# Performance work log

Hardware: AMD Instinct MI355X
Metric: run time of the kernel (lower is better)

The kernel has to match this reference:

```python
import jax, jax.numpy as jnp
import numpy as np


def setup_inputs() -> dict:
    key = jax.random.key(0)
    ks = jax.random.split(key, 8)
    B, M, C, H, W = 2, 16, 256, 64, 64
    T = 1024  # transformer_dim
    return {
        "transformer_output": jax.random.normal(ks[0], (B, T), dtype=jnp.float32),
        "residual_maps": jax.random.normal(ks[1], (B, M, C, H, W), dtype=jnp.float32),
        "Wq": jax.random.normal(ks[2], (C, T), dtype=jnp.float32) * 0.02,
        "bq": jnp.zeros((C,), dtype=jnp.float32),
        "Wk": jax.random.normal(ks[3], (C, C), dtype=jnp.float32) * 0.02,
        "bk": jnp.zeros((C,), dtype=jnp.float32),
        "Wv": jax.random.normal(ks[4], (C, C), dtype=jnp.float32) * 0.02,
        "bv": jnp.zeros((C,), dtype=jnp.float32),
    }


def reference(transformer_output, residual_maps, Wq, bq, Wk, bk, Wv, bv):
    # residual_maps: [B, M, C, H, W]; single query per batch element.
    B, M, C, H, W = residual_maps.shape
    scale = C ** (-0.5)
    # Linear query projection: [B, C]
    q = transformer_output @ Wq.T + bq
    # 1x1 conv == per-pixel channel matmul: [B, M, C, H, W]
    keys = jnp.einsum("oc,bmchw->bmohw", Wk, residual_maps) + bk[None, None, :, None, None]
    values = jnp.einsum("oc,bmchw->bmohw", Wv, residual_maps) + bv[None, None, :, None, None]
    # Single-query dot-product scores per (map, pixel): [B, M, H, W]
    scores = jnp.einsum("bc,bmchw->bmhw", q, keys) * scale
    # Temporal softmax over num_maps at each spatial position
    probs = jax.nn.softmax(scores, axis=1)
    # Softmax-weighted sum of value maps: [B, C, H, W]
    out = jnp.einsum("bmhw,bmchw->bchw", probs, values)
    return out
```

## Files before the change

kernel.cpp:

```cpp
#include <hip/hip_runtime.h>

#define SCALE 0.0625f

typedef __attribute__((ext_vector_type(4))) float f32x4;
typedef __attribute__((ext_vector_type(8))) short s16x8;

__device__ __forceinline__ unsigned short f2bf(float x) {
    unsigned u = __float_as_uint(x);
    u = u + 0x7FFF + ((u >> 16) & 1);
    return (unsigned short)(u >> 16);
}

__global__ __launch_bounds__(256) void prep1_kernel(
    const float* __restrict__ TO,
    const float* __restrict__ Wq,
    const float* __restrict__ bq,
    const float* __restrict__ Wv,
    float* __restrict__ qbuf,
    unsigned short* __restrict__ WvB)
{
    const int blk = blockIdx.x;
    const int t   = threadIdx.x;
    if (blk < 16) {
        const int b    = blk >> 3;
        const int rblk = blk & 7;
        const int wv = t >> 6, l = t & 63;
        const float4* Wq4 = (const float4*)Wq;
        const float4* TO4 = (const float4*)TO;
        for (int rr = 0; rr < 8; ++rr) {
            const int c = rblk * 32 + wv * 8 + rr;
            float acc = 0.f;
#pragma unroll
            for (int i = 0; i < 4; ++i) {
                float4 wq = Wq4[c * 256 + i * 64 + l];
                float4 tv = TO4[b * 256 + i * 64 + l];
                acc = fmaf(wq.x, tv.x, acc);
                acc = fmaf(wq.y, tv.y, acc);
                acc = fmaf(wq.z, tv.z, acc);
                acc = fmaf(wq.w, tv.w, acc);
            }
#pragma unroll
            for (int mask = 1; mask < 64; mask <<= 1)
                acc += __shfl_xor(acc, mask, 64);
            if (l == 0) qbuf[b * 256 + c] = acc + bq[c];
        }
    } else {
        const int idx = blk - 16;
#pragma unroll
        for (int i = 0; i < 4; ++i) {
            const int e = idx * 4096 + i * 1024 + t * 4;
            const float4 f = ((const float4*)Wv)[e >> 2];
            ushort4 o;
            o.x = f2bf(f.x); o.y = f2bf(f.y);
            o.z = f2bf(f.z); o.w = f2bf(f.w);
            *(ushort4*)(WvB + e) = o;
        }
    }
}

__global__ __launch_bounds__(256) void prep2_kernel(
    const float* __restrict__ qbuf,
    const float* __restrict__ Wk,
    float* __restrict__ qks)
{
    const int blk = blockIdx.x;
    const int t   = threadIdx.x;
    const int b = blk >> 3, j = blk & 7;
    const int col = t & 31, chunk = t >> 5;
    const int cp = j * 32 + col;
    float partial = 0.f;
#pragma unroll 8
    for (int cc = 0; cc < 32; ++cc) {
        const int c = chunk * 32 + cc;
        partial = fmaf(qbuf[b * 256 + c], Wk[c * 256 + cp], partial);
    }
    __shared__ float r2[8][32];
    r2[chunk][col] = partial;
    __syncthreads();
    if (t < 32) {
        float s = 0.f;
#pragma unroll
        for (int k = 0; k < 8; ++k) s += r2[k][t];
        qks[b * 256 + j * 32 + t] = SCALE * s;
    }
}

__global__ __launch_bounds__(64, 1) void main_kernel(
    const float* __restrict__ X,
    const float* __restrict__ qks,
    const unsigned short* __restrict__ WvB,
    const float* __restrict__ bv,
    float* __restrict__ out)
{
    const int t   = threadIdx.x;
    const int blk = blockIdx.x;
    const int pb  = ((blk & 7) << 6) | (blk >> 3);
    const int b   = pb >> 8;
    const int hw0 = (pb & 255) << 4;
    const int p4  = t & 3;
    const int cg  = t >> 2;

    __shared__ float slab[256 * 20];

    float qk[16];
#pragma unroll
    for (int k = 0; k < 16; ++k) qk[k] = qks[b * 256 + cg + 16 * k];

    const float4* X4 = (const float4*)X;
    const int base0 = (b * 16) * 262144 + (hw0 >> 2) + p4;

    float4 v[2][16];
    float4 wx[16];
#pragma unroll
    for (int k = 0; k < 16; ++k) wx[k] = make_float4(0.f, 0.f, 0.f, 0.f);
    float lsum[4] = {0.f, 0.f, 0.f, 0.f};

#pragma unroll
    for (int k = 0; k < 16; ++k)
        v[0][k] = X4[base0 + (cg + 16 * k) * 1024];

#pragma unroll
    for (int m = 0; m < 16; ++m) {
        const int buf = m & 1, nxt = buf ^ 1;
        if (m < 15) {
#pragma unroll
            for (int k = 0; k < 16; ++k)
                v[nxt][k] = X4[base0 + (m + 1) * 262144 + (cg + 16 * k) * 1024];
        }
        float sx = 0.f, sy = 0.f, sz = 0.f, sw = 0.f;
#pragma unroll
        for (int k = 0; k < 16; ++k) {
            sx = fmaf(qk[k], v[buf][k].x, sx);
            sy = fmaf(qk[k], v[buf][k].y, sy);
            sz = fmaf(qk[k], v[buf][k].z, sz);
            sw = fmaf(qk[k], v[buf][k].w, sw);
        }
#pragma unroll
        for (int mask = 4; mask < 64; mask <<= 1) {
            sx += __shfl_xor(sx, mask, 64);
            sy += __shfl_xor(sy, mask, 64);
            sz += __shfl_xor(sz, mask, 64);
            sw += __shfl_xor(sw, mask, 64);
        }
        const float w0 = __expf(sx), w1 = __expf(sy);
        const float w2 = __expf(sz), w3 = __expf(sw);
        lsum[0] += w0; lsum[1] += w1; lsum[2] += w2; lsum[3] += w3;
#pragma unroll
        for (int k = 0; k < 16; ++k) {
            wx[k].x = fmaf(w0, v[buf][k].x, wx[k].x);
            wx[k].y = fmaf(w1, v[buf][k].y, wx[k].y);
            wx[k].z = fmaf(w2, v[buf][k].z, wx[k].z);
            wx[k].w = fmaf(w3, v[buf][k].w, wx[k].w);
        }
    }

    const float i0 = 1.0f / lsum[0], i1 = 1.0f / lsum[1];
    const float i2 = 1.0f / lsum[2], i3 = 1.0f / lsum[3];
#pragma unroll
    for (int k = 0; k < 16; ++k) {
        *(float4*)&slab[(cg + 16 * k) * 20 + 4 * p4] =
            make_float4(wx[k].x * i0, wx[k].y * i1, wx[k].z * i2, wx[k].w * i3);
    }
    __syncthreads();

    const int px   = t & 15;
    const int quad = t >> 4;

    f32x4 acc[16];
#pragma unroll
    for (int tt = 0; tt < 16; ++tt) {
#pragma unroll
        for (int r = 0; r < 4; ++r)
            acc[tt][r] = bv[16 * tt + quad * 4 + r];
    }

#pragma unroll
    for (int ks = 0; ks < 8; ++ks) {
        s16x8 bfr;
#pragma unroll
        for (int j = 0; j < 8; ++j)
            bfr[j] = (short)f2bf(slab[(ks * 32 + quad * 8 + j) * 20 + px]);
#pragma unroll
        for (int tt = 0; tt < 16; ++tt) {
            const s16x8 afr =
                *(const s16x8*)(WvB + (16 * tt + px) * 256 + ks * 32 + quad * 8);
            acc[tt] = __builtin_amdgcn_mfma_f32_16x16x32_bf16(afr, bfr, acc[tt],
                                                              0, 0, 0);
        }
    }

    const int obase = b * 256 * 4096 + hw0;
#pragma unroll
    for (int tt = 0; tt < 16; ++tt) {
#pragma unroll
        for (int r = 0; r < 4; ++r) {
            const int co = 16 * tt + quad * 4 + r;
            out[obase + co * 4096 + px] = acc[tt][r];
        }
    }
}

extern "C" void kernel_launch(void* const* d_in, const int* in_sizes, int n_in,
                              void* d_out, int out_size, void* d_ws, size_t ws_size,
                              hipStream_t stream) {
    const float* TO = (const float*)d_in[0];
    const float* X  = (const float*)d_in[1];
    const float* Wq = (const float*)d_in[2];
    const float* bq = (const float*)d_in[3];
    const float* Wk = (const float*)d_in[4];
    const float* Wv = (const float*)d_in[6];
    const float* bv = (const float*)d_in[7];
    float* out = (float*)d_out;
    float* ws  = (float*)d_ws;

    float*          qbuf = ws;
    float*          qks  = ws + 512;
    unsigned short* WvB  = (unsigned short*)(ws + 1024);

    hipLaunchKernelGGL(prep1_kernel, dim3(32), dim3(256), 0, stream,
                       TO, Wq, bq, Wv, qbuf, WvB);
    hipLaunchKernelGGL(prep2_kernel, dim3(16), dim3(256), 0, stream,
                       qbuf, Wk, qks);
    hipLaunchKernelGGL(main_kernel, dim3(512), dim3(64), 0, stream,
                       X, qks, WvB, bv, out);
}
```

Before: 243.3 us.

## Split map loop across four waves per block and reduce partials in LDS

Each block now runs four wavefronts. Each wave handles four of the sixteen maps and keeps its own unnormalized weighted sums and exp sums. Wave 0 combines the partials through shared memory, normalizes them, and then all four waves share the MFMA value projection, four output tiles each. The aim is to raise memory-level parallelism and occupancy over the old single-wave serial loop across all maps. The cost is more LDS, two barriers and a cross-wave reduction. Skipping max subtraction in the exp is safe only because the exp sums are combined without rescaling, as before.

After: 244.8 us. Within noise of the previous version (+0.6%).

```diff
diff --git a/kernel.cpp b/kernel.cpp
--- a/kernel.cpp
+++ b/kernel.cpp
@@ -85,29 +85,35 @@
     }
 }
 
-__global__ __launch_bounds__(64, 1) void main_kernel(
+__global__ __launch_bounds__(256, 2) void main_kernel(
     const float* __restrict__ X,
     const float* __restrict__ qks,
     const unsigned short* __restrict__ WvB,
     const float* __restrict__ bv,
     float* __restrict__ out)
 {
-    const int t   = threadIdx.x;
-    const int blk = blockIdx.x;
-    const int pb  = ((blk & 7) << 6) | (blk >> 3);
-    const int b   = pb >> 8;
-    const int hw0 = (pb & 255) << 4;
-    const int p4  = t & 3;
-    const int cg  = t >> 2;
-
-    __shared__ float slab[256 * 20];
+    const int t    = threadIdx.x;
+    const int lane = t & 63;
+    const int w    = t >> 6;
+    const int blk  = blockIdx.x;
+    const int pb   = ((blk & 7) << 6) | (blk >> 3);
+    const int b    = pb >> 8;
+    const int hw0  = (pb & 255) << 4;
+    const int p4   = lane & 3;
+    const int cg   = lane >> 2;
+
+    __shared__ float smem[15360 + 64];
+    float* const s1    = smem;
+    float* const s2    = smem + 5120;
+    float* const slab  = smem + 10240;
+    float* const lsums = smem + 15360;
 
     float qk[16];
 #pragma unroll
     for (int k = 0; k < 16; ++k) qk[k] = qks[b * 256 + cg + 16 * k];
 
     const float4* X4 = (const float4*)X;
-    const int base0 = (b * 16) * 262144 + (hw0 >> 2) + p4;
+    const int base0 = (b * 16 + w * 4) * 262144 + (hw0 >> 2) + p4;
 
     float4 v[2][16];
     float4 wx[16];
@@ -120,12 +126,12 @@
         v[0][k] = X4[base0 + (cg + 16 * k) * 1024];
 
 #pragma unroll
-    for (int m = 0; m < 16; ++m) {
-        const int buf = m & 1, nxt = buf ^ 1;
-        if (m < 15) {
+    for (int i = 0; i < 4; ++i) {
+        const int buf = i & 1, nxt = buf ^ 1;
+        if (i < 3) {
 #pragma unroll
             for (int k = 0; k < 16; ++k)
-                v[nxt][k] = X4[base0 + (m + 1) * 262144 + (cg + 16 * k) * 1024];
+                v[nxt][k] = X4[base0 + (i + 1) * 262144 + (cg + 16 * k) * 1024];
         }
         float sx = 0.f, sy = 0.f, sz = 0.f, sw = 0.f;
 #pragma unroll
@@ -154,24 +160,53 @@
         }
     }
 
-    const float i0 = 1.0f / lsum[0], i1 = 1.0f / lsum[1];
-    const float i2 = 1.0f / lsum[2], i3 = 1.0f / lsum[3];
-#pragma unroll
-    for (int k = 0; k < 16; ++k) {
-        *(float4*)&slab[(cg + 16 * k) * 20 + 4 * p4] =
-            make_float4(wx[k].x * i0, wx[k].y * i1, wx[k].z * i2, wx[k].w * i3);
+    if (w != 0) {
+        float* dst = (w == 1) ? s1 : (w == 2) ? s2 : slab;
+#pragma unroll
+        for (int k = 0; k < 16; ++k)
+            *(float4*)&dst[(cg + 16 * k) * 20 + 4 * p4] = wx[k];
+    }
+    if (cg == 0) {
+#pragma unroll
+        for (int j = 0; j < 4; ++j) lsums[w * 16 + p4 * 4 + j] = lsum[j];
     }
     __syncthreads();
 
-    const int px   = t & 15;
-    const int quad = t >> 4;
-
-    f32x4 acc[16];
-#pragma unroll
-    for (int tt = 0; tt < 16; ++tt) {
+    if (w == 0) {
+        float inv[4];
+#pragma unroll
+        for (int j = 0; j < 4; ++j) {
+            const int px = p4 * 4 + j;
+            const float tot = lsums[px] + lsums[16 + px] +
+                              lsums[32 + px] + lsums[48 + px];
+            inv[j] = 1.0f / tot;
+        }
+#pragma unroll
+        for (int k = 0; k < 16; ++k) {
+            const int i = (cg + 16 * k) * 20 + 4 * p4;
+            const float4 a = *(const float4*)&s1[i];
+            const float4 c = *(const float4*)&s2[i];
+            const float4 d = *(const float4*)&slab[i];
+            float4 r;
+            r.x = (wx[k].x + a.x + c.x + d.x) * inv[0];
+            r.y = (wx[k].y + a.y + c.y + d.y) * inv[1];
+            r.z = (wx[k].z + a.z + c.z + d.z) * inv[2];
+            r.w = (wx[k].w + a.w + c.w + d.w) * inv[3];
+            *(float4*)&slab[i] = r;
+        }
+    }
+    __syncthreads();
+
+    const int px   = lane & 15;
+    const int quad = lane >> 4;
+
+    f32x4 acc[4];
+#pragma unroll
+    for (int tl = 0; tl < 4; ++tl) {
+        const int tt = w * 4 + tl;
 #pragma unroll
         for (int r = 0; r < 4; ++r)
-            acc[tt][r] = bv[16 * tt + quad * 4 + r];
+            acc[tl][r] = bv[16 * tt + quad * 4 + r];
     }
 
 #pragma unroll
@@ -181,21 +216,22 @@
         for (int j = 0; j < 8; ++j)
             bfr[j] = (short)f2bf(slab[(ks * 32 + quad * 8 + j) * 20 + px]);
 #pragma unroll
-        for (int tt = 0; tt < 16; ++tt) {
+        for (int tl = 0; tl < 4; ++tl) {
+            const int tt = w * 4 + tl;
             const s16x8 afr =
                 *(const s16x8*)(WvB + (16 * tt + px) * 256 + ks * 32 + quad * 8);
-            acc[tt] = __builtin_amdgcn_mfma_f32_16x16x32_bf16(afr, bfr, acc[tt],
+            acc[tl] = __builtin_amdgcn_mfma_f32_16x16x32_bf16(afr, bfr, acc[tl],
                                                               0, 0, 0);
         }
     }
 
     const int obase = b * 256 * 4096 + hw0;
 #pragma unroll
-    for (int tt = 0; tt < 16; ++tt) {
+    for (int tl = 0; tl < 4; ++tl) {
 #pragma unroll
         for (int r = 0; r < 4; ++r) {
-            const int co = 16 * tt + quad * 4 + r;
-            out[obase + co * 4096 + px] = acc[tt][r];
+            const int co = 16 * (w * 4 + tl) + quad * 4 + r;
+            out[obase + co * 4096 + px] = acc[tl][r];
         }
     }
 }
@@ -221,6 +257,6 @@
                        TO, Wq, bq, Wv, qbuf, WvB);
     hipLaunchKernelGGL(prep2_kernel, dim3(16), dim3(256), 0, stream,
                        qbuf, Wk, qks);
-    hipLaunchKernelGGL(main_kernel, dim3(512), dim3(64), 0, stream,
+    hipLaunchKernelGGL(main_kernel, dim3(512), dim3(256), 0, stream,
                        X, qks, WvB, bv, out);
 }
```

## Restructure main kernel into 512-thread blocks with LDS double-buffered map staging

Applied to the files above, without the earlier changes.

The main kernel moves from 512 single-wave blocks to 256 blocks of 8 waves, each covering 32 pixels. Each map is staged through a double-buffered shared-memory tile (padded rows), and each wave owns 4 pixels across all channels, which makes the score reduction a full-wave shuffle. The MFMA projection is split so each wave computes 32 output channels for both 16-pixel halves. The aim is more waves resident to hide global memory latency and less register pressure, at the cost of a barrier per map iteration and more LDS traffic.

Result: faster. 234.7 us (-3.5%).

```diff
diff --git a/kernel.cpp b/kernel.cpp
--- a/kernel.cpp
+++ b/kernel.cpp
@@ -1,6 +1,7 @@
 #include <hip/hip_runtime.h>
 
 #define SCALE 0.0625f
+#define ROW 36
 
 typedef __attribute__((ext_vector_type(4))) float f32x4;
 typedef __attribute__((ext_vector_type(8))) short s16x8;
@@ -85,119 +86,150 @@
     }
 }
 
-__global__ __launch_bounds__(64, 1) void main_kernel(
+__global__ __launch_bounds__(512, 2) void main_kernel(
     const float* __restrict__ X,
     const float* __restrict__ qks,
     const unsigned short* __restrict__ WvB,
     const float* __restrict__ bv,
     float* __restrict__ out)
 {
-    const int t   = threadIdx.x;
-    const int blk = blockIdx.x;
-    const int pb  = ((blk & 7) << 6) | (blk >> 3);
-    const int b   = pb >> 8;
-    const int hw0 = (pb & 255) << 4;
-    const int p4  = t & 3;
-    const int cg  = t >> 2;
-
-    __shared__ float slab[256 * 20];
-
-    float qk[16];
-#pragma unroll
-    for (int k = 0; k < 16; ++k) qk[k] = qks[b * 256 + cg + 16 * k];
-
+    const int t    = threadIdx.x;
+    const int lane = t & 63;
+    const int w    = t >> 6;
+    const int blk  = blockIdx.x;
+    const int b    = blk >> 7;
+    const int hw0  = (blk & 127) << 5;
+
+    __shared__ float lds[2 * 256 * ROW];
+    float* const buf0 = lds;
+    float* const buf1 = lds + 256 * ROW;
+
+    const int sc   = t >> 3;
+    const int spxq = t & 7;
     const float4* X4 = (const float4*)X;
-    const int base0 = (b * 16) * 262144 + (hw0 >> 2) + p4;
-
-    float4 v[2][16];
-    float4 wx[16];
-#pragma unroll
-    for (int k = 0; k < 16; ++k) wx[k] = make_float4(0.f, 0.f, 0.f, 0.f);
-    float lsum[4] = {0.f, 0.f, 0.f, 0.f};
-
-#pragma unroll
-    for (int k = 0; k < 16; ++k)
-        v[0][k] = X4[base0 + (cg + 16 * k) * 1024];
-
-#pragma unroll
+    const int gstage = b * 16 * 262144 + (hw0 >> 2) + spxq;
+
+    float qk[4];
+#pragma unroll
+    for (int c4 = 0; c4 < 4; ++c4)
+        qk[c4] = qks[b * 256 + lane + 64 * c4];
+
+    float4 wx[4];
+#pragma unroll
+    for (int c4 = 0; c4 < 4; ++c4) wx[c4] = make_float4(0.f, 0.f, 0.f, 0.f);
+    float lsx = 0.f, lsy = 0.f, lsz = 0.f, lsw = 0.f;
+
+    float4 sreg[4];
+#pragma unroll
+    for (int r = 0; r < 4; ++r)
+        sreg[r] = X4[gstage + 0 * 262144 + (sc + r * 64) * 1024];
+#pragma unroll
+    for (int r = 0; r < 4; ++r)
+        *(float4*)&buf0[(sc + r * 64) * ROW + spxq * 4] = sreg[r];
+
+#pragma unroll 2
     for (int m = 0; m < 16; ++m) {
-        const int buf = m & 1, nxt = buf ^ 1;
+        __syncthreads();
+        float* const cur  = (m & 1) ? buf1 : buf0;
+        float* const nxtb = (m & 1) ? buf0 : buf1;
+
         if (m < 15) {
 #pragma unroll
-            for (int k = 0; k < 16; ++k)
-                v[nxt][k] = X4[base0 + (m + 1) * 262144 + (cg + 16 * k) * 1024];
-        }
+            for (int r = 0; r < 4; ++r)
+                sreg[r] = X4[gstage + (m + 1) * 262144 + (sc + r * 64) * 1024];
+        }
+
+        float4 v[4];
+#pragma unroll
+        for (int c4 = 0; c4 < 4; ++c4)
+            v[c4] = *(const float4*)&cur[(lane + 64 * c4) * ROW + w * 4];
+
         float sx = 0.f, sy = 0.f, sz = 0.f, sw = 0.f;
 #pragma unroll
-        for (int k = 0; k < 16; ++k) {
-            sx = fmaf(qk[k], v[buf][k].x, sx);
-            sy = fmaf(qk[k], v[buf][k].y, sy);
-            sz = fmaf(qk[k], v[buf][k].z, sz);
-            sw = fmaf(qk[k], v[buf][k].w, sw);
-        }
-#pragma unroll
-        for (int mask = 4; mask < 64; mask <<= 1) {
+        for (int c4 = 0; c4 < 4; ++c4) {
+            sx = fmaf(qk[c4], v[c4].x, sx);
+            sy = fmaf(qk[c4], v[c4].y, sy);
+            sz = fmaf(qk[c4], v[c4].z, sz);
+            sw = fmaf(qk[c4], v[c4].w, sw);
+        }
+#pragma unroll
+        for (int mask = 1; mask < 64; mask <<= 1) {
             sx += __shfl_xor(sx, mask, 64);
             sy += __shfl_xor(sy, mask, 64);
             sz += __shfl_xor(sz, mask, 64);
             sw += __shfl_xor(sw, mask, 64);
         }
-        const float w0 = __expf(sx), w1 = __expf(sy);
-        const float w2 = __expf(sz), w3 = __expf(sw);
-        lsum[0] += w0; lsum[1] += w1; lsum[2] += w2; lsum[3] += w3;
-#pragma unroll
-        for (int k = 0; k < 16; ++k) {
-            wx[k].x = fmaf(w0, v[buf][k].x, wx[k].x);
-            wx[k].y = fmaf(w1, v[buf][k].y, wx[k].y);
-            wx[k].z = fmaf(w2, v[buf][k].z, wx[k].z);
-            wx[k].w = fmaf(w3, v[buf][k].w, wx[k].w);
-        }
-    }
-
-    const float i0 = 1.0f / lsum[0], i1 = 1.0f / lsum[1];
-    const float i2 = 1.0f / lsum[2], i3 = 1.0f / lsum[3];
-#pragma unroll
-    for (int k = 0; k < 16; ++k) {
-        *(float4*)&slab[(cg + 16 * k) * 20 + 4 * p4] =
-            make_float4(wx[k].x * i0, wx[k].y * i1, wx[k].z * i2, wx[k].w * i3);
+        const float e0 = __expf(sx), e1 = __expf(sy);
+        const float e2 = __expf(sz), e3 = __expf(sw);
+        lsx += e0; lsy += e1; lsz += e2; lsw += e3;
+#pragma unroll
+        for (int c4 = 0; c4 < 4; ++c4) {
+            wx[c4].x = fmaf(e0, v[c4].x, wx[c4].x);
+            wx[c4].y = fmaf(e1, v[c4].y, wx[c4].y);
+            wx[c4].z = fmaf(e2, v[c4].z, wx[c4].z);
+            wx[c4].w = fmaf(e3, v[c4].w, wx[c4].w);
+        }
+
+        if (m < 15) {
+#pragma unroll
+            for (int r = 0; r < 4; ++r)
+                *(float4*)&nxtb[(sc + r * 64) * ROW + spxq * 4] = sreg[r];
+        }
+    }
+
+    const float i0 = 1.0f / lsx, i1 = 1.0f / lsy;
+    const float i2 = 1.0f / lsz, i3 = 1.0f / lsw;
+#pragma unroll
+    for (int c4 = 0; c4 < 4; ++c4) {
+        float4 r;
+        r.x = wx[c4].x * i0; r.y = wx[c4].y * i1;
+        r.z = wx[c4].z * i2; r.w = wx[c4].w * i3;
+        *(float4*)&buf0[(lane + 64 * c4) * ROW + w * 4] = r;
     }
     __syncthreads();
 
-    const int px   = t & 15;
-    const int quad = t >> 4;
-
-    f32x4 acc[16];
-#pragma unroll
-    for (int tt = 0; tt < 16; ++tt) {
-#pragma unroll
-        for (int r = 0; r < 4; ++r)
-            acc[tt][r] = bv[16 * tt + quad * 4 + r];
-    }
+    const int px16 = lane & 15;
+    const int quad = lane >> 4;
+
+    f32x4 acc[2][2];
+#pragma unroll
+    for (int tl = 0; tl < 2; ++tl)
+#pragma unroll
+        for (int pxh = 0; pxh < 2; ++pxh)
+#pragma unroll
+            for (int r = 0; r < 4; ++r)
+                acc[tl][pxh][r] = bv[16 * (w * 2 + tl) + quad * 4 + r];
 
 #pragma unroll
     for (int ks = 0; ks < 8; ++ks) {
-        s16x8 bfr;
-#pragma unroll
-        for (int j = 0; j < 8; ++j)
-            bfr[j] = (short)f2bf(slab[(ks * 32 + quad * 8 + j) * 20 + px]);
-#pragma unroll
-        for (int tt = 0; tt < 16; ++tt) {
-            const s16x8 afr =
-                *(const s16x8*)(WvB + (16 * tt + px) * 256 + ks * 32 + quad * 8);
-            acc[tt] = __builtin_amdgcn_mfma_f32_16x16x32_bf16(afr, bfr, acc[tt],
-                                                              0, 0, 0);
+        s16x8 bfr[2];
+#pragma unroll
+        for (int pxh = 0; pxh < 2; ++pxh)
+#pragma unroll
+            for (int j = 0; j < 8; ++j)
+                bfr[pxh][j] = (short)f2bf(
+                    buf0[(ks * 32 + quad * 8 + j) * ROW + pxh * 16 + px16]);
+#pragma unroll
+        for (int tl = 0; tl < 2; ++tl) {
+            const s16x8 afr = *(const s16x8*)(
+                WvB + (16 * (w * 2 + tl) + px16) * 256 + ks * 32 + quad * 8);
+#pragma unroll
+            for (int pxh = 0; pxh < 2; ++pxh)
+                acc[tl][pxh] = __builtin_amdgcn_mfma_f32_16x16x32_bf16(
+                    afr, bfr[pxh], acc[tl][pxh], 0, 0, 0);
         }
     }
 
     const int obase = b * 256 * 4096 + hw0;
 #pragma unroll
-    for (int tt = 0; tt < 16; ++tt) {
-#pragma unroll
-        for (int r = 0; r < 4; ++r) {
-            const int co = 16 * tt + quad * 4 + r;
-            out[obase + co * 4096 + px] = acc[tt][r];
-        }
-    }
+    for (int tl = 0; tl < 2; ++tl)
+#pragma unroll
+        for (int pxh = 0; pxh < 2; ++pxh)
+#pragma unroll
+            for (int r = 0; r < 4; ++r) {
+                const int co = 16 * (w * 2 + tl) + quad * 4 + r;
+                out[obase + co * 4096 + pxh * 16 + px16] = acc[tl][pxh][r];
+            }
 }
 
 extern "C" void kernel_launch(void* const* d_in, const int* in_sizes, int n_in,
@@ -221,6 +253,6 @@
                        TO, Wq, bq, Wv, qbuf, WvB);
     hipLaunchKernelGGL(prep2_kernel, dim3(16), dim3(256), 0, stream,
                        qbuf, Wk, qks);
-    hipLaunchKernelGGL(main_kernel, dim3(512), dim3(64), 0, stream,
+    hipLaunchKernelGGL(main_kernel, dim3(256), dim3(512), 0, stream,
                        X, qks, WvB, bv, out);
 }
```
